# Kernel tuning notes

Measured on AMD Instinct MI355X. Metric: run time of the kernel, lower is better.

The kernel has to match this reference:

```python
import jax, jax.numpy as jnp
import numpy as np
import math

B, T, DIM = 4, 2048, 1024
N_HEADS, HEAD_DIM = 8, 128
WINDOW = 16
EPS = 1e-6
NEG = -1e9

def _alibi_slopes(n_heads):
    # n_heads=8 is a power of 2
    r = 2.0 ** (-8.0 / n_heads)
    return jnp.asarray([r ** i for i in range(n_heads)], dtype=jnp.float32)

def _rms_norm(x, w, eps):
    var = jnp.mean(jnp.square(x), axis=-1, keepdims=True)
    return x * jax.lax.rsqrt(var + eps) * w

def setup_inputs() -> dict:
    key = jax.random.key(0)
    ks = jax.random.split(key, 7)
    s = 1.0 / math.sqrt(DIM)
    return {
        "x": jax.random.normal(ks[0], (B, T, DIM), dtype=jnp.float32),
        # weights stored as [in, out]; apply as x @ W
        "wq": jax.random.normal(ks[1], (DIM, N_HEADS * HEAD_DIM), dtype=jnp.float32) * s,
        "wk": jax.random.normal(ks[2], (DIM, N_HEADS * HEAD_DIM), dtype=jnp.float32) * s,
        "wv": jax.random.normal(ks[3], (DIM, N_HEADS * HEAD_DIM), dtype=jnp.float32) * s,
        "wo": jax.random.normal(ks[4], (N_HEADS * HEAD_DIM, DIM), dtype=jnp.float32) * s,
        "q_norm_w": jnp.ones((N_HEADS * HEAD_DIM,), dtype=jnp.float32),
        "k_norm_w": jnp.ones((N_HEADS * HEAD_DIM,), dtype=jnp.float32),
    }

def reference(x, wq, wk, wv, wo, q_norm_w, k_norm_w):
    Bx, Tx, _ = x.shape
    xq = _rms_norm(x @ wq, q_norm_w, EPS)
    xk = _rms_norm(x @ wk, k_norm_w, EPS)
    xv = x @ wv
    # [B, H, T, D]
    q = xq.reshape(Bx, Tx, N_HEADS, HEAD_DIM).transpose(0, 2, 1, 3)
    k = xk.reshape(Bx, Tx, N_HEADS, HEAD_DIM).transpose(0, 2, 1, 3)
    v = xv.reshape(Bx, Tx, N_HEADS, HEAD_DIM).transpose(0, 2, 1, 3)

    pos = jnp.arange(Tx)
    rel = pos[None, :] - pos[:, None]            # rel[i, j] = j - i
    slopes = _alibi_slopes(N_HEADS)
    bias = slopes[:, None, None] * rel.astype(jnp.float32)  # [H, T, T]
    # causal (j > i) and sliding-window (j < i - WINDOW) masked
    invalid = (rel > 0) | (rel < -WINDOW)
    bias = jnp.where(invalid[None, :, :], NEG, bias)

    scale = 1.0 / math.sqrt(HEAD_DIM)
    scores = jnp.einsum("bhqd,bhkd->bhqk", q, k) * scale + bias[None]
    probs = jax.nn.softmax(scores, axis=-1)
    y = jnp.einsum("bhqk,bhkd->bhqd", probs, v)
    y = y.transpose(0, 2, 1, 3).reshape(Bx, Tx, N_HEADS * HEAD_DIM)
    return y @ wo
```

## Files before the change

kernel.cpp:

```cpp
#include <hip/hip_runtime.h>
#include <hip/hip_bf16.h>
#include <math.h>


#define TSEQ 2048
#define DIMW 1024
#define NHEAD 8
#define WIN 16

typedef __bf16 bf16x8_t __attribute__((ext_vector_type(8)));
typedef float f32x4_t __attribute__((ext_vector_type(4)));

__device__ __forceinline__ unsigned short f2bf(float f) {
  unsigned u = __float_as_uint(f);
  u += 0x7fffu + ((u >> 16) & 1u);
  return (unsigned short)(u >> 16);
}
__device__ __forceinline__ float bflo(unsigned u) { return __uint_as_float(u << 16); }
__device__ __forceinline__ float bfhi(unsigned u) { return __uint_as_float(u & 0xffff0000u); }

__global__ __launch_bounds__(256)
void k_conv_x(const float* __restrict__ x, unsigned short* __restrict__ xb, int n4) {
  int i = blockIdx.x * 256 + threadIdx.x;
  if (i >= n4) return;
  float4 v = ((const float4*)x)[i];
  ushort4 o;
  o.x = f2bf(v.x); o.y = f2bf(v.y); o.z = f2bf(v.z); o.w = f2bf(v.w);
  ((ushort4*)xb)[i] = o;
}

__global__ __launch_bounds__(256)
void k_conv_w(const float* __restrict__ wq, const float* __restrict__ wk,
              const float* __restrict__ wv, const float* __restrict__ wo,
              unsigned short* __restrict__ Wt) {
  __shared__ float tile[32][33];
  const int z = blockIdx.z;
  const float* src = (z == 0) ? wq : (z == 1) ? wk : (z == 2) ? wv : wo;
  const int n0 = blockIdx.x * 32;
  const int k0 = blockIdx.y * 32;
  const int tx = threadIdx.x, ty = threadIdx.y;
#pragma unroll
  for (int i = 0; i < 4; ++i)
    tile[ty + 8 * i][tx] = src[(size_t)(k0 + ty + 8 * i) * DIMW + n0 + tx];
  __syncthreads();
#pragma unroll
  for (int i = 0; i < 4; ++i)
    Wt[(size_t)z * DIMW * DIMW + (size_t)(n0 + ty + 8 * i) * DIMW + k0 + tx] =
        f2bf(tile[tx][ty + 8 * i]);
}

#define GLDS(gp, lp)                                                        \
  __builtin_amdgcn_global_load_lds(                                         \
      (const __attribute__((address_space(1))) void*)(gp),                  \
      (__attribute__((address_space(3))) void*)(lp), 16, 0, 0)

template <int MODE>
__global__ __launch_bounds__(256, 3)
void k_gemm(const unsigned short* __restrict__ A,
            const unsigned short* __restrict__ Bt,
            unsigned short* __restrict__ Cb,
            unsigned short* __restrict__ Vt,
            float* __restrict__ Cf,
            int M, int N, int K) {
  __shared__ __align__(16) unsigned char smem[49152];
  const int tid = threadIdx.x;
  const int lane = tid & 63;
  const int w = tid >> 6;
  const int wm = w >> 1, wn = w & 1;

  const int nwg = gridDim.x * gridDim.y;
  int flat = blockIdx.y * gridDim.x + blockIdx.x;
  flat = (flat & 7) * (nwg >> 3) + (flat >> 3);
  const int bx = flat % gridDim.x;
  const int by = flat / gridDim.x;

  const int r2 = lane >> 2;
  const int cg = ((lane & 3) ^ ((lane >> 3) & 3)) * 8;

#define IA(sl_, ks_, h_)                                                       \
  GLDS(A + (size_t)(by * 128 + (h_)*64 + w * 16 + r2) * K + (ks_)*32 + cg,     \
       smem + (sl_)*16384 + ((h_)*64 + w * 16) * 64)
#define IB(sl_, ks_, h_)                                                       \
  GLDS(Bt + (size_t)(bx * 128 + (h_)*64 + w * 16 + r2) * K + (ks_)*32 + cg,    \
       smem + (sl_)*16384 + 8192 + ((h_)*64 + w * 16) * 64)
#define STAGE(ks_)                                                             \
  do {                                                                         \
    const int sl_ = (ks_) % 3;                                                 \
    IA(sl_, (ks_), 0); IB(sl_, (ks_), 0);                                      \
    IA(sl_, (ks_), 1); IB(sl_, (ks_), 1);                                      \
  } while (0)

  const int swz = ((lane >> 4) ^ ((lane >> 1) & 3)) * 16;
  const int aRd = (wm * 64 + (lane & 15)) * 64 + swz;
  const int bRd = 8192 + (wn * 64 + (lane & 15)) * 64 + swz;

  f32x4_t acc[4][4];
#pragma unroll
  for (int m = 0; m < 4; ++m)
#pragma unroll
    for (int n = 0; n < 4; ++n) acc[m][n] = (f32x4_t){0.f, 0.f, 0.f, 0.f};

  const int NS = K >> 5;
  STAGE(0); STAGE(1);
#pragma unroll 1
  for (int s = 0; s < NS; ++s) {
    if (s + 1 < NS) asm volatile("s_waitcnt vmcnt(4)" ::: "memory");
    else            asm volatile("s_waitcnt vmcnt(0)" ::: "memory");
    asm volatile("s_barrier" ::: "memory");
    if (s + 2 < NS) STAGE(s + 2);
    const unsigned char* sp = smem + (s % 3) * 16384;
    bf16x8_t af[4], bfr[4];
#pragma unroll
    for (int n = 0; n < 4; ++n) bfr[n] = *(const bf16x8_t*)(sp + bRd + n * 1024);
#pragma unroll
    for (int m = 0; m < 4; ++m) af[m] = *(const bf16x8_t*)(sp + aRd + m * 1024);
    __builtin_amdgcn_s_setprio(1);
#pragma unroll
    for (int m = 0; m < 4; ++m)
#pragma unroll
      for (int n = 0; n < 4; ++n)
        acc[m][n] = __builtin_amdgcn_mfma_f32_16x16x32_bf16(af[m], bfr[n], acc[m][n], 0, 0, 0);
    __builtin_amdgcn_s_setprio(0);
  }

  const int g = lane >> 4, c = lane & 15;
  if (MODE == 1) {
    const int row0 = by * 128 + wm * 64 + (g << 2);
    const int col0 = bx * 128 + wn * 64 + c;
#pragma unroll
    for (int m = 0; m < 4; ++m)
#pragma unroll
      for (int n = 0; n < 4; ++n)
#pragma unroll
        for (int r = 0; r < 4; ++r)
          Cf[(size_t)(row0 + m * 16 + r) * N + col0 + n * 16] = acc[m][n][r];
  } else {
    __syncthreads();
    unsigned short* wbuf = (unsigned short*)(smem + w * 9216);
    const bool isV = (bx * 128 >= 2048);
#pragma unroll
    for (int m = 0; m < 4; ++m)
#pragma unroll
      for (int n = 0; n < 4; ++n)
#pragma unroll
        for (int r = 0; r < 4; ++r) {
          const int rl = m * 16 + (g << 2) + r;
          const int cl = n * 16 + c;
          const unsigned short v = f2bf(acc[m][n][r]);
          if (isV) wbuf[cl * 72 + rl] = v;
          else     wbuf[rl * 72 + cl] = v;
        }
    if (!isV) {
      const int grow = by * 128 + wm * 64;
      const int gcol = bx * 128 + wn * 64;
#pragma unroll
      for (int rr = 0; rr < 8; ++rr) {
        const int row = rr * 8 + (lane >> 3);
        const int seg = lane & 7;
        uint4 u;
        __builtin_memcpy(&u, wbuf + row * 72 + seg * 8, 16);
        *(uint4*)(Cb + (size_t)(grow + row) * 2048 + gcol + seg * 8) = u;
      }
    } else {
      const int tt0 = (by * 128 + wm * 64) & 2047;
      const int bb = (by * 128) >> 11;
      const int hh = bx - 16;
      const int dd0 = wn * 64;
      unsigned short* vdst =
          Vt + ((((size_t)(bb * NHEAD + hh)) * 256 + (tt0 >> 3)) * 128 + dd0 + lane) * 8;
#pragma unroll
      for (int tc = 0; tc < 8; ++tc) {
        uint4 u;
        __builtin_memcpy(&u, wbuf + lane * 72 + tc * 8, 16);
        *(uint4*)(vdst + (size_t)tc * 1024) = u;
      }
    }
  }
#undef IA
#undef IB
#undef STAGE
}

__global__ __launch_bounds__(256)
void k_rmsnorm(unsigned short* __restrict__ qk, const float* __restrict__ qw,
               const float* __restrict__ kw) {
  const int row = blockIdx.x;
  const int tid = threadIdx.x;
  unsigned short* base = qk + (size_t)row * 2048;
  uint2 uq = *(const uint2*)(base + tid * 4);
  uint2 uk = *(const uint2*)(base + 1024 + tid * 4);
  float q0 = bflo(uq.x), q1 = bfhi(uq.x), q2 = bflo(uq.y), q3 = bfhi(uq.y);
  float k0 = bflo(uk.x), k1 = bfhi(uk.x), k2 = bflo(uk.y), k3 = bfhi(uk.y);
  float sq = q0 * q0 + q1 * q1 + q2 * q2 + q3 * q3;
  float sk = k0 * k0 + k1 * k1 + k2 * k2 + k3 * k3;
#pragma unroll
  for (int off = 32; off > 0; off >>= 1) {
    sq += __shfl_xor(sq, off);
    sk += __shfl_xor(sk, off);
  }
  __shared__ float red[8];
  const int w = tid >> 6;
  if ((tid & 63) == 0) { red[w] = sq; red[4 + w] = sk; }
  __syncthreads();
  sq = red[0] + red[1] + red[2] + red[3];
  sk = red[4] + red[5] + red[6] + red[7];
  const float rq = rsqrtf(sq * (1.0f / 1024.0f) + 1e-6f);
  const float rk = rsqrtf(sk * (1.0f / 1024.0f) + 1e-6f);
  const int c = tid * 4;
  uint2 oq, ok;
  oq.x = (unsigned)f2bf(q0 * rq * qw[c]) | ((unsigned)f2bf(q1 * rq * qw[c + 1]) << 16);
  oq.y = (unsigned)f2bf(q2 * rq * qw[c + 2]) | ((unsigned)f2bf(q3 * rq * qw[c + 3]) << 16);
  ok.x = (unsigned)f2bf(k0 * rk * kw[c]) | ((unsigned)f2bf(k1 * rk * kw[c + 1]) << 16);
  ok.y = (unsigned)f2bf(k2 * rk * kw[c + 2]) | ((unsigned)f2bf(k3 * rk * kw[c + 3]) << 16);
  *(uint2*)(base + tid * 4) = oq;
  *(uint2*)(base + 1024 + tid * 4) = ok;
}

__global__ __launch_bounds__(256)
void k_attn(const unsigned short* __restrict__ qk,
            const unsigned short* __restrict__ vt,
            unsigned short* __restrict__ outb) {
  __shared__ __align__(16) unsigned char plds_all[4][1280];
  __shared__ __align__(16) unsigned short obuf_all[4][16 * 136];
  const int lane = threadIdx.x & 63;
  const int wv = threadIdx.x >> 6;
  unsigned char* plds = plds_all[wv];
  unsigned short* obuf = obuf_all[wv];
  const int bh = blockIdx.y;
  const int b = bh >> 3, h = bh & 7;
  const int t0 = blockIdx.x * 64 + wv * 16;
  const int g = lane >> 4, c = lane & 15;
  const int jlo = t0 - 16;

  const unsigned short* qrow = qk + (size_t)(b * TSEQ + t0 + c) * 2048 + h * 128 + g * 8;
  bf16x8_t qf[4];
#pragma unroll
  for (int kc = 0; kc < 4; ++kc) qf[kc] = *(const bf16x8_t*)(qrow + kc * 32);

  const int j0 = jlo + c;
  const int j0c = (j0 < 0) ? 0 : j0;
  const unsigned short* krow0 = qk + (size_t)(b * TSEQ + j0c) * 2048 + 1024 + h * 128 + g * 8;
  const unsigned short* krow1 = qk + (size_t)(b * TSEQ + t0 + c) * 2048 + 1024 + h * 128 + g * 8;
  bf16x8_t kf0[4], kf1[4];
#pragma unroll
  for (int kc = 0; kc < 4; ++kc) {
    kf0[kc] = *(const bf16x8_t*)(krow0 + kc * 32);
    kf1[kc] = *(const bf16x8_t*)(krow1 + kc * 32);
  }

  int tc = (jlo >> 3) + g;
  if (tc < 0) tc = 0;
  const unsigned short* vbase = vt + (((size_t)bh * 256 + tc) * 128 + c) * 8;
  bf16x8_t vf[8];
#pragma unroll
  for (int n = 0; n < 8; ++n) vf[n] = *(const bf16x8_t*)(vbase + n * 128);

  f32x4_t s0 = (f32x4_t){0.f, 0.f, 0.f, 0.f};
  f32x4_t s1 = (f32x4_t){0.f, 0.f, 0.f, 0.f};
#pragma unroll
  for (int kc = 0; kc < 4; ++kc) {
    s0 = __builtin_amdgcn_mfma_f32_16x16x32_bf16(kf0[kc], qf[kc], s0, 0, 0, 0);
    s1 = __builtin_amdgcn_mfma_f32_16x16x32_bf16(kf1[kc], qf[kc], s1, 0, 0, 0);
  }

  const float scale = 0.08838834764831845f;
  const float slope = 1.0f / (float)(1 << h);
  float val[8];
#pragma unroll
  for (int z = 0; z < 2; ++z)
#pragma unroll
    for (int r = 0; r < 4; ++r) {
      const int kk = z * 16 + g * 4 + r;
      const int rel = kk - 16 - c;
      const bool ok = (rel <= 0) & (rel >= -WIN) & (jlo + kk >= 0);
      const float sc = (z == 0) ? s0[r] : s1[r];
      val[z * 4 + r] = ok ? (sc * scale + slope * (float)rel) : -1.0e30f;
    }
  float m = val[0];
#pragma unroll
  for (int i = 1; i < 8; ++i) m = fmaxf(m, val[i]);
  m = fmaxf(m, __shfl_xor(m, 16));
  m = fmaxf(m, __shfl_xor(m, 32));
  float e[8], s = 0.f;
#pragma unroll
  for (int i = 0; i < 8; ++i) { e[i] = __expf(val[i] - m); s += e[i]; }
  s += __shfl_xor(s, 16);
  s += __shfl_xor(s, 32);
  const float inv = 1.0f / s;

#pragma unroll
  for (int z = 0; z < 2; ++z) {
    uint2 pk;
    pk.x = (unsigned)f2bf(e[z * 4 + 0] * inv) | ((unsigned)f2bf(e[z * 4 + 1] * inv) << 16);
    pk.y = (unsigned)f2bf(e[z * 4 + 2] * inv) | ((unsigned)f2bf(e[z * 4 + 3] * inv) << 16);
    *(uint2*)(plds + c * 80 + z * 32 + g * 8) = pk;
  }
  const bf16x8_t pf = *(const bf16x8_t*)(plds + c * 80 + g * 16);

#pragma unroll
  for (int n = 0; n < 8; ++n) {
    f32x4_t o = __builtin_amdgcn_mfma_f32_16x16x32_bf16(pf, vf[n], (f32x4_t){0.f, 0.f, 0.f, 0.f},
                                                        0, 0, 0);
#pragma unroll
    for (int r = 0; r < 4; ++r)
      obuf[(g * 4 + r) * 136 + n * 16 + c] = f2bf(o[r]);
  }

  unsigned short* obase = outb + (size_t)(b * TSEQ + t0) * 1024 + h * 128;
  const int q = lane >> 2, s4 = lane & 3;
#pragma unroll
  for (int i = 0; i < 4; ++i) {
    const int seg = i * 4 + s4;
    uint4 u;
    __builtin_memcpy(&u, obuf + q * 136 + seg * 8, 16);
    *(uint4*)(obase + (size_t)q * 1024 + seg * 8) = u;
  }
}

extern "C" void kernel_launch(void* const* d_in, const int* in_sizes, int n_in,
                              void* d_out, int out_size, void* d_ws, size_t ws_size,
                              hipStream_t stream) {
  const float* x = (const float*)d_in[0];
  const float* wq = (const float*)d_in[1];
  const float* wk = (const float*)d_in[2];
  const float* wv = (const float*)d_in[3];
  const float* wo = (const float*)d_in[4];
  const float* qnw = (const float*)d_in[5];
  const float* knw = (const float*)d_in[6];
  float* out = (float*)d_out;

  const int M = 4 * TSEQ;
  unsigned short* xb = (unsigned short*)d_ws;
  unsigned short* Wt = xb + (size_t)M * DIMW;
  unsigned short* qkb = Wt + (size_t)4 * DIMW * DIMW;
  unsigned short* Vt = qkb + (size_t)M * 2048;
  if (ws_size < ((size_t)M * DIMW + (size_t)4 * DIMW * DIMW + (size_t)M * 2048 +
                 (size_t)M * 2048) * 2) return;

  k_conv_x<<<(M * DIMW / 4 + 255) / 256, 256, 0, stream>>>(x, xb, M * DIMW / 4);
  k_conv_w<<<dim3(32, 32, 4), dim3(32, 8), 0, stream>>>(wq, wk, wv, wo, Wt);
  k_gemm<0><<<dim3(24, 64), 256, 0, stream>>>(xb, Wt, qkb, Vt, nullptr, M, 3072, 1024);
  k_rmsnorm<<<M, 256, 0, stream>>>(qkb, qnw, knw);
  k_attn<<<dim3(TSEQ / 64, 32), 256, 0, stream>>>(qkb, Vt, xb);
  k_gemm<1><<<dim3(8, 64), 256, 0, stream>>>(xb, Wt + (size_t)3 * DIMW * DIMW, nullptr,
                                             nullptr, out, M, 1024, 1024);
}
```

Baseline: 216.2 us.

## Fuse RMSNorm into QKV GEMM epilogue and attention, merge prep kernels

```diff
diff --git a/kernel.cpp b/kernel.cpp
--- a/kernel.cpp
+++ b/kernel.cpp
@@ -20,33 +20,40 @@
 __device__ __forceinline__ float bfhi(unsigned u) { return __uint_as_float(u & 0xffff0000u); }
 
 __global__ __launch_bounds__(256)
-void k_conv_x(const float* __restrict__ x, unsigned short* __restrict__ xb, int n4) {
-  int i = blockIdx.x * 256 + threadIdx.x;
-  if (i >= n4) return;
-  float4 v = ((const float4*)x)[i];
-  ushort4 o;
-  o.x = f2bf(v.x); o.y = f2bf(v.y); o.z = f2bf(v.z); o.w = f2bf(v.w);
-  ((ushort4*)xb)[i] = o;
-}
-
-__global__ __launch_bounds__(256)
-void k_conv_w(const float* __restrict__ wq, const float* __restrict__ wk,
-              const float* __restrict__ wv, const float* __restrict__ wo,
-              unsigned short* __restrict__ Wt) {
-  __shared__ float tile[32][33];
-  const int z = blockIdx.z;
-  const float* src = (z == 0) ? wq : (z == 1) ? wk : (z == 2) ? wv : wo;
-  const int n0 = blockIdx.x * 32;
-  const int k0 = blockIdx.y * 32;
-  const int tx = threadIdx.x, ty = threadIdx.y;
-#pragma unroll
-  for (int i = 0; i < 4; ++i)
-    tile[ty + 8 * i][tx] = src[(size_t)(k0 + ty + 8 * i) * DIMW + n0 + tx];
-  __syncthreads();
-#pragma unroll
-  for (int i = 0; i < 4; ++i)
-    Wt[(size_t)z * DIMW * DIMW + (size_t)(n0 + ty + 8 * i) * DIMW + k0 + tx] =
-        f2bf(tile[tx][ty + 8 * i]);
+void k_prep(const float* __restrict__ x, const float* __restrict__ wq,
+            const float* __restrict__ wk, const float* __restrict__ wv,
+            const float* __restrict__ wo, unsigned short* __restrict__ xb,
+            unsigned short* __restrict__ Wt, float* __restrict__ norms) {
+  const int blk = blockIdx.x;
+  const int tid = threadIdx.x;
+  if (blk < 8192) {
+    const int i = blk * 256 + tid;
+    float4 v = ((const float4*)x)[i];
+    ushort4 o;
+    o.x = f2bf(v.x); o.y = f2bf(v.y); o.z = f2bf(v.z); o.w = f2bf(v.w);
+    ((ushort4*)xb)[i] = o;
+  } else if (blk < 12288) {
+    __shared__ float tile[32][33];
+    const int zi = blk - 8192;
+    const int z = zi >> 10;
+    const float* src = (z == 0) ? wq : (z == 1) ? wk : (z == 2) ? wv : wo;
+    const int idx = zi & 1023;
+    const int n0 = (idx & 31) * 32;
+    const int k0 = (idx >> 5) * 32;
+    const int tx = tid & 31, ty = tid >> 5;
+#pragma unroll
+    for (int i = 0; i < 4; ++i)
+      tile[ty + 8 * i][tx] = src[(size_t)(k0 + ty + 8 * i) * DIMW + n0 + tx];
+    __syncthreads();
+#pragma unroll
+    for (int i = 0; i < 4; ++i)
+      Wt[(size_t)z * DIMW * DIMW + (size_t)(n0 + ty + 8 * i) * DIMW + k0 + tx] =
+          f2bf(tile[tx][ty + 8 * i]);
+  } else {
+    const int i = (blk - 12288) * 512 + tid * 2;
+    norms[i] = 0.f;
+    norms[i + 1] = 0.f;
+  }
 }
 
 #define GLDS(gp, lp)                                                        \
@@ -61,6 +68,7 @@
             unsigned short* __restrict__ Cb,
             unsigned short* __restrict__ Vt,
             float* __restrict__ Cf,
+            float* __restrict__ norms,
             int M, int N, int K) {
   __shared__ __align__(16) unsigned char smem[49152];
   const int tid = threadIdx.x;
@@ -135,9 +143,26 @@
         for (int r = 0; r < 4; ++r)
           Cf[(size_t)(row0 + m * 16 + r) * N + col0 + n * 16] = acc[m][n][r];
   } else {
+    const bool isV = (bx * 128 >= 2048);
+    if (!isV) {
+      const int half = (bx < 8) ? 0 : 1;
+      const int rbase = by * 128 + wm * 64 + (g << 2);
+#pragma unroll
+      for (int m = 0; m < 4; ++m)
+#pragma unroll
+        for (int r = 0; r < 4; ++r) {
+          float ss = 0.f;
+#pragma unroll
+          for (int n = 0; n < 4; ++n) { const float v = acc[m][n][r]; ss += v * v; }
+          ss += __shfl_xor(ss, 1);
+          ss += __shfl_xor(ss, 2);
+          ss += __shfl_xor(ss, 4);
+          ss += __shfl_xor(ss, 8);
+          if (c == 0) atomicAdd(norms + (size_t)(rbase + m * 16 + r) * 2 + half, ss);
+        }
+    }
     __syncthreads();
     unsigned short* wbuf = (unsigned short*)(smem + w * 9216);
-    const bool isV = (bx * 128 >= 2048);
 #pragma unroll
     for (int m = 0; m < 4; ++m)
 #pragma unroll
@@ -181,44 +206,23 @@
 #undef STAGE
 }
 
-__global__ __launch_bounds__(256)
-void k_rmsnorm(unsigned short* __restrict__ qk, const float* __restrict__ qw,
-               const float* __restrict__ kw) {
-  const int row = blockIdx.x;
-  const int tid = threadIdx.x;
-  unsigned short* base = qk + (size_t)row * 2048;
-  uint2 uq = *(const uint2*)(base + tid * 4);
-  uint2 uk = *(const uint2*)(base + 1024 + tid * 4);
-  float q0 = bflo(uq.x), q1 = bfhi(uq.x), q2 = bflo(uq.y), q3 = bfhi(uq.y);
-  float k0 = bflo(uk.x), k1 = bfhi(uk.x), k2 = bflo(uk.y), k3 = bfhi(uk.y);
-  float sq = q0 * q0 + q1 * q1 + q2 * q2 + q3 * q3;
-  float sk = k0 * k0 + k1 * k1 + k2 * k2 + k3 * k3;
-#pragma unroll
-  for (int off = 32; off > 0; off >>= 1) {
-    sq += __shfl_xor(sq, off);
-    sk += __shfl_xor(sk, off);
-  }
-  __shared__ float red[8];
-  const int w = tid >> 6;
-  if ((tid & 63) == 0) { red[w] = sq; red[4 + w] = sk; }
-  __syncthreads();
-  sq = red[0] + red[1] + red[2] + red[3];
-  sk = red[4] + red[5] + red[6] + red[7];
-  const float rq = rsqrtf(sq * (1.0f / 1024.0f) + 1e-6f);
-  const float rk = rsqrtf(sk * (1.0f / 1024.0f) + 1e-6f);
-  const int c = tid * 4;
-  uint2 oq, ok;
-  oq.x = (unsigned)f2bf(q0 * rq * qw[c]) | ((unsigned)f2bf(q1 * rq * qw[c + 1]) << 16);
-  oq.y = (unsigned)f2bf(q2 * rq * qw[c + 2]) | ((unsigned)f2bf(q3 * rq * qw[c + 3]) << 16);
-  ok.x = (unsigned)f2bf(k0 * rk * kw[c]) | ((unsigned)f2bf(k1 * rk * kw[c + 1]) << 16);
-  ok.y = (unsigned)f2bf(k2 * rk * kw[c + 2]) | ((unsigned)f2bf(k3 * rk * kw[c + 3]) << 16);
-  *(uint2*)(base + tid * 4) = oq;
-  *(uint2*)(base + 1024 + tid * 4) = ok;
+__device__ __forceinline__ bf16x8_t scale8(bf16x8_t v, const float* __restrict__ wp,
+                                           float r) {
+  bf16x8_t o;
+#pragma unroll
+  for (int j = 0; j < 8; ++j) {
+    const float f = (float)v[j] * (r * wp[j]);
+    o[j] = (__bf16)f;
+  }
+  return o;
 }
 
 __global__ __launch_bounds__(256)
 void k_attn(const unsigned short* __restrict__ qk,
             const unsigned short* __restrict__ vt,
+            const float* __restrict__ norms,
+            const float* __restrict__ qnw,
+            const float* __restrict__ knw,
             unsigned short* __restrict__ outb) {
   __shared__ __align__(16) unsigned char plds_all[4][1280];
   __shared__ __align__(16) unsigned short obuf_all[4][16 * 136];
@@ -255,6 +259,20 @@
 #pragma unroll
   for (int n = 0; n < 8; ++n) vf[n] = *(const bf16x8_t*)(vbase + n * 128);
 
+  const float inv1024 = 1.0f / 1024.0f;
+  const float rq  = rsqrtf(norms[(size_t)(b * TSEQ + t0 + c) * 2 + 0] * inv1024 + 1e-6f);
+  const float rk0 = rsqrtf(norms[(size_t)(b * TSEQ + j0c) * 2 + 1] * inv1024 + 1e-6f);
+  const float rk1 = rsqrtf(norms[(size_t)(b * TSEQ + t0 + c) * 2 + 1] * inv1024 + 1e-6f);
+
+#pragma unroll
+  for (int kc = 0; kc < 4; ++kc) {
+    const float* qwp = qnw + h * 128 + kc * 32 + g * 8;
+    const float* kwp = knw + h * 128 + kc * 32 + g * 8;
+    qf[kc] = scale8(qf[kc], qwp, rq);
+    kf0[kc] = scale8(kf0[kc], kwp, rk0);
+    kf1[kc] = scale8(kf1[kc], kwp, rk1);
+  }
+
   f32x4_t s0 = (f32x4_t){0.f, 0.f, 0.f, 0.f};
   f32x4_t s1 = (f32x4_t){0.f, 0.f, 0.f, 0.f};
 #pragma unroll
@@ -334,14 +352,13 @@
   unsigned short* Wt = xb + (size_t)M * DIMW;
   unsigned short* qkb = Wt + (size_t)4 * DIMW * DIMW;
   unsigned short* Vt = qkb + (size_t)M * 2048;
+  float* norms = (float*)(Vt + (size_t)M * 1024);
   if (ws_size < ((size_t)M * DIMW + (size_t)4 * DIMW * DIMW + (size_t)M * 2048 +
-                 (size_t)M * 2048) * 2) return;
-
-  k_conv_x<<<(M * DIMW / 4 + 255) / 256, 256, 0, stream>>>(x, xb, M * DIMW / 4);
-  k_conv_w<<<dim3(32, 32, 4), dim3(32, 8), 0, stream>>>(wq, wk, wv, wo, Wt);
-  k_gemm<0><<<dim3(24, 64), 256, 0, stream>>>(xb, Wt, qkb, Vt, nullptr, M, 3072, 1024);
-  k_rmsnorm<<<M, 256, 0, stream>>>(qkb, qnw, knw);
-  k_attn<<<dim3(TSEQ / 64, 32), 256, 0, stream>>>(qkb, Vt, xb);
+                 (size_t)M * 1024) * 2 + (size_t)M * 2 * 4) return;
+
+  k_prep<<<12320, 256, 0, stream>>>(x, wq, wk, wv, wo, xb, Wt, norms);
+  k_gemm<0><<<dim3(24, 64), 256, 0, stream>>>(xb, Wt, qkb, Vt, nullptr, norms, M, 3072, 1024);
+  k_attn<<<dim3(TSEQ / 64, 32), 256, 0, stream>>>(qkb, Vt, norms, qnw, knw, xb);
   k_gemm<1><<<dim3(8, 64), 256, 0, stream>>>(xb, Wt + (size_t)3 * DIMW * DIMW, nullptr,
-                                             nullptr, out, M, 1024, 1024);
-}
+                                             nullptr, out, nullptr, M, 1024, 1024);
+}
```

Result: no change. 212.4 us (-1.8%).
